# Kernel tuning notes

Measured on AMD Instinct MI355X. Metric: run time of the kernel, lower is better.

The kernel has to match this reference:

```python
import jax, jax.numpy as jnp
import numpy as np

B, S, D, DK = 8, 2048, 768, 214
DROPOUT_P = 0.1


def setup_inputs() -> dict:
    key = jax.random.key(0)
    ks = jax.random.split(key, 11)
    x1 = jax.random.normal(ks[0], (B, S, D), jnp.float32)
    x2 = jax.random.normal(ks[1], (B, S, D), jnp.float32)
    x3 = jax.random.normal(ks[2], (B, S, D), jnp.float32)
    Wq = jax.random.normal(ks[3], (DK, D), jnp.float32) * (1.0 / np.sqrt(D))
    bq = jax.random.normal(ks[4], (DK,), jnp.float32) * 0.01
    Wk = jax.random.normal(ks[5], (DK, D), jnp.float32) * (1.0 / np.sqrt(D))
    bk = jax.random.normal(ks[6], (DK,), jnp.float32) * 0.01
    Wv = jax.random.normal(ks[7], (D, D), jnp.float32) * (1.0 / np.sqrt(D))
    bv = jax.random.normal(ks[8], (D,), jnp.float32) * 0.01
    # full-tensor elementwise divisor: uniform(0,1) + 1, as in the source
    inv_scale = jax.random.uniform(ks[9], (S, S), jnp.float32) + 1.0
    # deterministic inverted-dropout mask, keep prob = 1 - p
    keep = 1.0 - DROPOUT_P
    dropout_mask = (jax.random.uniform(ks[10], (B, S, S)) < keep).astype(jnp.float32) / keep
    return dict(x1=x1, x2=x2, x3=x3, Wq=Wq, bq=bq, Wk=Wk, bk=bk,
                Wv=Wv, bv=bv, inv_scale=inv_scale, dropout_mask=dropout_mask)


def reference(x1, x2, x3, Wq, bq, Wk, bk, Wv, bv, inv_scale, dropout_mask):
    q = jnp.einsum('bsd,kd->bsk', x1, Wq) + bq          # [B,S,DK]
    k = jnp.einsum('bsd,kd->bsk', x2, Wk) + bk          # [B,S,DK]
    v = jnp.einsum('bsd,ed->bse', x3, Wv) + bv          # [B,S,D]
    attn = jnp.einsum('bsk,btk->bst', q, k)             # [B,S,S]
    scaled = attn / inv_scale                           # elementwise full-tensor divisor
    p = jax.nn.softmax(scaled, axis=-1) * dropout_mask  # softmax + inverted dropout
    return jnp.einsum('bst,btd->bsd', p, v)             # [B,S,D]
```

## Files before the change

kernel.cpp:

```cpp
#include <hip/hip_runtime.h>
#include <hip/hip_bf16.h>

typedef unsigned short ushort;
typedef short bf16x8 __attribute__((ext_vector_type(8)));
typedef float f32x4 __attribute__((ext_vector_type(4)));

#define NB 8
#define SS 2048
#define DD 768
#define DKV 214
#define DKP 224
#define WROWS 256
#define MSHIFT 40.0f

__device__ __forceinline__ float bf2f(ushort u) {
  union { unsigned int i; float f; } v; v.i = ((unsigned int)u) << 16; return v.f;
}
__device__ __forceinline__ ushort f2bf(float f) {
  union { float f; unsigned int i; } v; v.f = f;
  unsigned int x = v.i;
  return (ushort)((x + 0x7fffu + ((x >> 16) & 1u)) >> 16);
}
__device__ __forceinline__ void split8v(f32x4 a, f32x4 b, bf16x8& h, bf16x8& l) {
#pragma unroll
  for (int j = 0; j < 4; ++j) {
    ushort h0 = f2bf(a[j]); h[j]     = (short)h0; l[j]     = (short)f2bf(a[j] - bf2f(h0));
    ushort h1 = f2bf(b[j]); h[j + 4] = (short)h1; l[j + 4] = (short)f2bf(b[j] - bf2f(h1));
  }
}
__device__ __forceinline__ bf16x8 cvt8v(f32x4 a, f32x4 b) {
  bf16x8 r;
#pragma unroll
  for (int j = 0; j < 4; ++j) { r[j] = (short)f2bf(a[j]); r[j + 4] = (short)f2bf(b[j]); }
  return r;
}
__device__ __forceinline__ void gload16(const void* g, void* l) {
  __builtin_amdgcn_global_load_lds(
      (const __attribute__((address_space(1))) void*)g,
      (__attribute__((address_space(3))) void*)l, 16, 0, 0);
}

__global__ __launch_bounds__(256)
void prep_w(const float* __restrict__ Wq, const float* __restrict__ Wk,
            const float* __restrict__ Wv,
            ushort* __restrict__ Wqh, ushort* __restrict__ Wql,
            ushort* __restrict__ Wkh, ushort* __restrict__ Wkl,
            ushort* __restrict__ Wvb, float* __restrict__ Z)
{
  const int NW = WROWS * DD;
  const int NV = DD * DD;
  for (int i = blockIdx.x * 256 + threadIdx.x; i < NB * SS; i += gridDim.x * 256)
    Z[i] = 0.f;
  for (int i = blockIdx.x * 256 + threadIdx.x; i < 2 * NW + NV; i += gridDim.x * 256) {
    if (i < NW) {
      int r = i / DD, c = i % DD;
      float v = (r < DKV) ? Wq[i] : 0.f;
      ushort h = f2bf(v);
      int d = (c >> 5) * (WROWS * 32) + r * 32 + (c & 31);
      Wqh[d] = h; Wql[d] = f2bf(v - bf2f(h));
    } else if (i < 2 * NW) {
      int j = i - NW;
      int r = j / DD, c = j % DD;
      float v = (r < DKV) ? Wk[j] : 0.f;
      ushort h = f2bf(v);
      int d = (c >> 5) * (WROWS * 32) + r * 32 + (c & 31);
      Wkh[d] = h; Wkl[d] = f2bf(v - bf2f(h));
    } else {
      int j = i - 2 * NW;
      int r = j / DD, c = j % DD;
      Wvb[(c >> 5) * (DD * 32) + r * 32 + (c & 31)] = f2bf(Wv[j]);
    }
  }
}

__global__ __launch_bounds__(256, 4)
void gemm_qk(const float* __restrict__ x1, const float* __restrict__ x2,
             const ushort* __restrict__ Wqh, const ushort* __restrict__ Wql,
             const ushort* __restrict__ Wkh, const ushort* __restrict__ Wkl,
             const float* __restrict__ bq, const float* __restrict__ bk,
             ushort* __restrict__ Qph, ushort* __restrict__ Qpl,
             ushort* __restrict__ Kph, ushort* __restrict__ Kpl)
{
  const int m0 = blockIdx.x * 64;
  const int which = blockIdx.y >> 1;
  const int n0 = (blockIdx.y & 1) * 128;
  const int tid = threadIdx.x;
  const int w  = tid >> 6;
  const int l  = tid & 63;
  const int lr = l & 15;
  const int lh = l >> 4;

  const float*  A    = which ? x2 : x1;
  const ushort* Bh   = which ? Wkh : Wqh;
  const ushort* Bl   = which ? Wkl : Wql;
  const float*  bias = which ? bk : bq;
  ushort* Ch = which ? Kph : Qph;
  ushort* Cl = which ? Kpl : Qpl;

  __shared__ __align__(16) char lds[2][2][128][64];

  const int srow = (w << 4) + (l >> 2);
  const size_t gc = (size_t)srow * 64 + (size_t)((((l & 3) ^ ((srow >> 1) & 3))) << 4);
  const char* gbh = (const char*)Bh + (size_t)n0 * 64;
  const char* gbl = (const char*)Bl + (size_t)n0 * 64;

  const f32x4 fzero = {0.f, 0.f, 0.f, 0.f};
  f32x4 acc[8];
#pragma unroll
  for (int nt = 0; nt < 8; ++nt) acc[nt] = fzero;

  const float* arow = A + (size_t)(m0 + w * 16 + lr) * DD + lh * 8;

#define QKSTAGE(buf, kk) do {                                             \
    size_t ko = (size_t)(kk) * (WROWS * 64);                              \
    gload16(gbh + ko + gc,        &lds[buf][0][w << 4][0]);               \
    gload16(gbh + ko + gc + 4096, &lds[buf][0][(w << 4) + 64][0]);        \
    gload16(gbl + ko + gc,        &lds[buf][1][w << 4][0]);               \
    gload16(gbl + ko + gc + 4096, &lds[buf][1][(w << 4) + 64][0]);        \
  } while (0)

  QKSTAGE(0, 0);
  f32x4 pa = *(const f32x4*)(arow);
  f32x4 pb = *(const f32x4*)(arow + 4);
  __syncthreads();

  for (int kk = 0; kk < 24; ++kk) {
    const int buf = kk & 1;
    if (kk < 23) QKSTAGE(buf ^ 1, kk + 1);
    f32x4 na = fzero, nb = fzero;
    if (kk < 23) {
      na = *(const f32x4*)(arow + (kk + 1) * 32);
      nb = *(const f32x4*)(arow + (kk + 1) * 32 + 4);
    }
    bf16x8 ah, al; split8v(pa, pb, ah, al);
#pragma unroll
    for (int nt = 0; nt < 8; ++nt) {
      int br = nt * 16 + lr;
      int bo = (lh ^ ((br >> 1) & 3)) << 4;
      bf16x8 wh = *(const bf16x8*)&lds[buf][0][br][bo];
      bf16x8 wl = *(const bf16x8*)&lds[buf][1][br][bo];
      acc[nt] = __builtin_amdgcn_mfma_f32_16x16x32_bf16(ah, wh, acc[nt], 0, 0, 0);
      acc[nt] = __builtin_amdgcn_mfma_f32_16x16x32_bf16(ah, wl, acc[nt], 0, 0, 0);
      acc[nt] = __builtin_amdgcn_mfma_f32_16x16x32_bf16(al, wh, acc[nt], 0, 0, 0);
    }
    __syncthreads();
    pa = na; pb = nb;
  }
#undef QKSTAGE

#pragma unroll
  for (int nt = 0; nt < 8; ++nt) {
    int n = n0 + nt * 16 + lr;
    if (n >= DKP) continue;
    float bv = (n < DKV) ? bias[n] : 0.f;
#pragma unroll
    for (int r = 0; r < 4; ++r) {
      int m = m0 + w * 16 + lh * 4 + r;
      int bb = m >> 11, s = m & 2047;
      float val = (n < DKV) ? (acc[nt][r] + bv) : 0.f;
      ushort h = f2bf(val);
      size_t idx = ((size_t)(bb * 7 + (n >> 5)) * SS + s) * 32 + (n & 31);
      Ch[idx] = h;
      Cl[idx] = f2bf(val - bf2f(h));
    }
  }
}

__global__ __launch_bounds__(256, 3)
void gemm_v(const float* __restrict__ A, const ushort* __restrict__ Bw,
            const float* __restrict__ bias, ushort* __restrict__ Vp)
{
  const int m0 = blockIdx.x * 64;
  const int n0 = blockIdx.y * 256;
  const int tid = threadIdx.x;
  const int w  = tid >> 6;
  const int l  = tid & 63;
  const int lr = l & 15;
  const int lh = l >> 4;

  __shared__ __align__(16) char smem[36864];
  typedef char VBuf[256][64];
  VBuf* stage = (VBuf*)smem;
  ushort (*lt)[72] = (ushort(*)[72])smem;

  const int srow = (w << 4) + (l >> 2);
  const size_t gc = (size_t)srow * 64 + (size_t)((((l & 3) ^ ((srow >> 1) & 3))) << 4);
  const char* gvw = (const char*)Bw + (size_t)n0 * 64;

  const f32x4 fzero = {0.f, 0.f, 0.f, 0.f};
  f32x4 acc[16];
#pragma unroll
  for (int nt = 0; nt < 16; ++nt) acc[nt] = fzero;

  const float* arow = A + (size_t)(m0 + w * 16 + lr) * DD + lh * 8;

#define VSTAGE(buf, kk) do {                                              \
    size_t ko = (size_t)(kk) * (DD * 64);                                 \
    gload16(gvw + ko + gc,         &stage[buf][w << 4][0]);               \
    gload16(gvw + ko + gc + 4096,  &stage[buf][(w << 4) + 64][0]);        \
    gload16(gvw + ko + gc + 8192,  &stage[buf][(w << 4) + 128][0]);       \
    gload16(gvw + ko + gc + 12288, &stage[buf][(w << 4) + 192][0]);       \
  } while (0)

  VSTAGE(0, 0);
  f32x4 pa = *(const f32x4*)(arow);
  f32x4 pb = *(const f32x4*)(arow + 4);
  __syncthreads();

  for (int kk = 0; kk < 24; ++kk) {
    const int buf = kk & 1;
    if (kk < 23) VSTAGE(buf ^ 1, kk + 1);
    f32x4 na = fzero, nb = fzero;
    if (kk < 23) {
      na = *(const f32x4*)(arow + (kk + 1) * 32);
      nb = *(const f32x4*)(arow + (kk + 1) * 32 + 4);
    }
    bf16x8 af = cvt8v(pa, pb);
#pragma unroll
    for (int nt = 0; nt < 16; ++nt) {
      int br = nt * 16 + lr;
      int bo = (lh ^ ((br >> 1) & 3)) << 4;
      bf16x8 bfr = *(const bf16x8*)&stage[buf][br][bo];
      acc[nt] = __builtin_amdgcn_mfma_f32_16x16x32_bf16(af, bfr, acc[nt], 0, 0, 0);
    }
    __syncthreads();
    pa = na; pb = nb;
  }
#undef VSTAGE

#pragma unroll
  for (int nt = 0; nt < 16; ++nt) {
    int nl = nt * 16 + lr;
    float bv = bias[n0 + nl];
#pragma unroll
    for (int r = 0; r < 4; ++r)
      lt[nl][w * 16 + lh * 4 + r] = f2bf(acc[nt][r] + bv);
  }
  __syncthreads();
  const int bb = m0 >> 11;
  const int s0 = m0 & 2047;
  for (int i = tid; i < 256 * 64; i += 256) {
    int nn = i >> 6, mm = i & 63;
    int d = n0 + nn, t = s0 + mm;
    Vp[((size_t)(bb * 64 + (t >> 5)) * DD + d) * 32 + (t & 31)] = lt[nn][mm];
  }
}

__global__ __launch_bounds__(512, 4)
void gemm_s(const ushort* __restrict__ Qph, const ushort* __restrict__ Qpl,
            const ushort* __restrict__ Kph, const ushort* __restrict__ Kpl,
            const float* __restrict__ isc, const float* __restrict__ dmask,
            ushort* __restrict__ Pp, float* __restrict__ Z)
{
  const int bid = blockIdx.x;
  const int bb = bid & 7;
  const int tt = bid >> 3;
  const int m0 = (tt & 15) * 128;
  const int n0 = (tt >> 4) * 256;
  const int tid = threadIdx.x;
  const int w  = tid >> 6;
  const int l  = tid & 63;
  const int lr = l & 15;
  const int lh = l >> 4;
  const int wm = w & 1;
  const int wn = w >> 1;

  __shared__ __align__(16) char Qhb[128][64];
  __shared__ __align__(16) char Qlb[128][64];
  __shared__ __align__(16) char Khb[256][64];
  __shared__ __align__(16) char Klb[256][64];

  const int srow = (w << 4) + (l >> 2);
  const size_t gc = (size_t)srow * 64 + (size_t)((((l & 3) ^ ((srow >> 1) & 3))) << 4);

  const char* gqh = (const char*)Qph + ((size_t)(bb * 7) * SS + m0) * 64;
  const char* gql = (const char*)Qpl + ((size_t)(bb * 7) * SS + m0) * 64;
  const char* gkh = (const char*)Kph + ((size_t)(bb * 7) * SS + n0) * 64;
  const char* gkl = (const char*)Kpl + ((size_t)(bb * 7) * SS + n0) * 64;

  const f32x4 fzero = {0.f, 0.f, 0.f, 0.f};
  f32x4 acc[4][4];
#pragma unroll
  for (int mf = 0; mf < 4; ++mf)
#pragma unroll
    for (int nf = 0; nf < 4; ++nf) acc[mf][nf] = fzero;

#define SSTAGE(kk) do {                                                 \
    size_t ko = (size_t)(kk) * (SS * 64);                               \
    gload16(gqh + ko + gc,        &Qhb[w << 4][0]);                     \
    gload16(gql + ko + gc,        &Qlb[w << 4][0]);                     \
    gload16(gkh + ko + gc,        &Khb[w << 4][0]);                     \
    gload16(gkh + ko + gc + 8192, &Khb[(w << 4) + 128][0]);             \
    gload16(gkl + ko + gc,        &Klb[w << 4][0]);                     \
    gload16(gkl + ko + gc + 8192, &Klb[(w << 4) + 128][0]);             \
  } while (0)

  SSTAGE(0);
  __syncthreads();
#pragma unroll 1
  for (int t = 0; t < 7; ++t) {
    bf16x8 bh[4], bl[4];
#pragma unroll
    for (int nf = 0; nf < 4; ++nf) {
      int br = wn * 64 + nf * 16 + lr;
      int bo = (lh ^ ((br >> 1) & 3)) << 4;
      bh[nf] = *(const bf16x8*)&Khb[br][bo];
      bl[nf] = *(const bf16x8*)&Klb[br][bo];
    }
#pragma unroll
    for (int mf = 0; mf < 4; ++mf) {
      int ar = wm * 64 + mf * 16 + lr;
      int ao = (lh ^ ((ar >> 1) & 3)) << 4;
      bf16x8 ah = *(const bf16x8*)&Qhb[ar][ao];
      bf16x8 al = *(const bf16x8*)&Qlb[ar][ao];
#pragma unroll
      for (int nf = 0; nf < 4; ++nf) {
        acc[mf][nf] = __builtin_amdgcn_mfma_f32_16x16x32_bf16(ah, bh[nf], acc[mf][nf], 0, 0, 0);
        acc[mf][nf] = __builtin_amdgcn_mfma_f32_16x16x32_bf16(ah, bl[nf], acc[mf][nf], 0, 0, 0);
        acc[mf][nf] = __builtin_amdgcn_mfma_f32_16x16x32_bf16(al, bh[nf], acc[mf][nf], 0, 0, 0);
      }
    }
    __syncthreads();
    if (t < 6) {
      SSTAGE(t + 1);
      __syncthreads();
    }
  }
#undef SSTAGE

#pragma unroll
  for (int mf = 0; mf < 4; ++mf) {
#pragma unroll
    for (int r = 0; r < 4; ++r) {
      const int sr = m0 + wm * 64 + mf * 16 + lh * 4 + r;
      float z = 0.f;
#pragma unroll
      for (int nf = 0; nf < 4; ++nf) {
        const int tc = n0 + wn * 64 + nf * 16 + lr;
        float iv = isc[(size_t)sr * SS + tc];
        float sval = acc[mf][nf][r] * __builtin_amdgcn_rcpf(iv);
        float e = __expf(sval - MSHIFT);
        z += e;
        float mk = dmask[(size_t)bb * SS * SS + (size_t)sr * SS + tc];
        Pp[((size_t)(bb * 64 + (tc >> 5)) * SS + sr) * 32 + (tc & 31)] = f2bf(e * mk);
      }
#pragma unroll
      for (int off = 1; off < 16; off <<= 1) z += __shfl_xor(z, off);
      if (lr == 0) atomicAdd(&Z[bb * SS + sr], z);
    }
  }
}

__global__ __launch_bounds__(256, 4)
void gemm_pv(const ushort* __restrict__ Pp, const ushort* __restrict__ Vp,
             const float* __restrict__ Z, float* __restrict__ out)
{
  const int bid = blockIdx.x;
  const int bb = bid & 7;
  const int tt = bid >> 3;
  const int m0 = (tt & 15) * 128;
  const int n0 = (tt >> 4) * 128;
  const int tid = threadIdx.x;
  const int w  = tid >> 6;
  const int l  = tid & 63;
  const int lr = l & 15;
  const int lh = l >> 4;
  const int wm = w & 1;
  const int wn = w >> 1;

  __shared__ __align__(16) char Plb[2][128][64];
  __shared__ __align__(16) char Vlb[2][128][64];

  const int srow = (w << 4) + (l >> 2);
  const size_t gc = (size_t)srow * 64 + (size_t)((((l & 3) ^ ((srow >> 1) & 3))) << 4);

  const char* gpb = (const char*)Pp + ((size_t)(bb * 64) * SS + m0) * 64;
  const char* gvb = (const char*)Vp + ((size_t)(bb * 64) * DD + n0) * 64;

  const f32x4 fzero = {0.f, 0.f, 0.f, 0.f};
  f32x4 acc[4][4];
#pragma unroll
  for (int mf = 0; mf < 4; ++mf)
#pragma unroll
    for (int nf = 0; nf < 4; ++nf) acc[mf][nf] = fzero;

#define PVSTAGE(t) do {                                                   \
    size_t k0 = (size_t)(t) * 2;                                          \
    gload16(gpb + k0 * (SS * 64) + gc,              &Plb[0][w << 4][0]);  \
    gload16(gpb + k0 * (SS * 64) + gc + 4096,       &Plb[0][(w << 4) + 64][0]); \
    gload16(gpb + (k0 + 1) * (SS * 64) + gc,        &Plb[1][w << 4][0]);  \
    gload16(gpb + (k0 + 1) * (SS * 64) + gc + 4096, &Plb[1][(w << 4) + 64][0]); \
    gload16(gvb + k0 * (DD * 64) + gc,              &Vlb[0][w << 4][0]);  \
    gload16(gvb + k0 * (DD * 64) + gc + 4096,       &Vlb[0][(w << 4) + 64][0]); \
    gload16(gvb + (k0 + 1) * (DD * 64) + gc,        &Vlb[1][w << 4][0]);  \
    gload16(gvb + (k0 + 1) * (DD * 64) + gc + 4096, &Vlb[1][(w << 4) + 64][0]); \
  } while (0)

  PVSTAGE(0);
  __syncthreads();
#pragma unroll 1
  for (int t = 0; t < 32; ++t) {
#pragma unroll
    for (int pk = 0; pk < 2; ++pk) {
      bf16x8 bfr[4];
#pragma unroll
      for (int nf = 0; nf < 4; ++nf) {
        int br = wn * 64 + nf * 16 + lr;
        int bo = (lh ^ ((br >> 1) & 3)) << 4;
        bfr[nf] = *(const bf16x8*)&Vlb[pk][br][bo];
      }
#pragma unroll
      for (int mf = 0; mf < 4; ++mf) {
        int ar = wm * 64 + mf * 16 + lr;
        int ao = (lh ^ ((ar >> 1) & 3)) << 4;
        bf16x8 af = *(const bf16x8*)&Plb[pk][ar][ao];
#pragma unroll
        for (int nf = 0; nf < 4; ++nf)
          acc[mf][nf] = __builtin_amdgcn_mfma_f32_16x16x32_bf16(af, bfr[nf], acc[mf][nf], 0, 0, 0);
      }
    }
    __syncthreads();
    if (t < 31) {
      PVSTAGE(t + 1);
      __syncthreads();
    }
  }
#undef PVSTAGE

#pragma unroll
  for (int mf = 0; mf < 4; ++mf) {
#pragma unroll
    for (int r = 0; r < 4; ++r) {
      const int sr = m0 + wm * 64 + mf * 16 + lh * 4 + r;
      float rz = __builtin_amdgcn_rcpf(Z[bb * SS + sr]);
#pragma unroll
      for (int nf = 0; nf < 4; ++nf) {
        const int dc = n0 + wn * 64 + nf * 16 + lr;
        out[((size_t)bb * SS + sr) * DD + dc] = acc[mf][nf][r] * rz;
      }
    }
  }
}

extern "C" void kernel_launch(void* const* d_in, const int* in_sizes, int n_in,
                              void* d_out, int out_size, void* d_ws, size_t ws_size,
                              hipStream_t stream) {
  const float* x1  = (const float*)d_in[0];
  const float* x2  = (const float*)d_in[1];
  const float* x3  = (const float*)d_in[2];
  const float* Wq  = (const float*)d_in[3];
  const float* bq  = (const float*)d_in[4];
  const float* Wk  = (const float*)d_in[5];
  const float* bk  = (const float*)d_in[6];
  const float* Wv  = (const float*)d_in[7];
  const float* bv  = (const float*)d_in[8];
  const float* isc = (const float*)d_in[9];
  const float* dmk = (const float*)d_in[10];
  float* out = (float*)d_out;

  const size_t QKN = (size_t)NB * 7 * SS * 32;
  const size_t VPN = (size_t)NB * 64 * DD * 32;
  const size_t WN  = (size_t)WROWS * DD;
  const size_t NV  = (size_t)DD * DD;
  const size_t PPN = (size_t)NB * 64 * SS * 32;

  ushort* Qph = (ushort*)d_ws;
  ushort* Qpl = Qph + QKN;
  ushort* Kph = Qpl + QKN;
  ushort* Kpl = Kph + QKN;
  ushort* Vp  = Kpl + QKN;
  ushort* Wqh = Vp + VPN;
  ushort* Wql = Wqh + WN;
  ushort* Wkh = Wql + WN;
  ushort* Wkl = Wkh + WN;
  ushort* Wvb = Wkl + WN;
  ushort* Pp  = Wvb + NV;
  float*  Zb  = (float*)(Pp + PPN);

  dim3 blk(256);
  prep_w<<<dim3(512), blk, 0, stream>>>(Wq, Wk, Wv, Wqh, Wql, Wkh, Wkl, Wvb, Zb);
  gemm_qk<<<dim3(256, 4), blk, 0, stream>>>(x1, x2, Wqh, Wql, Wkh, Wkl, bq, bk,
                                            Qph, Qpl, Kph, Kpl);
  gemm_v <<<dim3(256, 3), blk, 0, stream>>>(x3, Wvb, bv, Vp);
  gemm_s <<<dim3(1024), dim3(512), 0, stream>>>(Qph, Qpl, Kph, Kpl, isc, dmk, Pp, Zb);
  gemm_pv<<<dim3(768),  dim3(256), 0, stream>>>(Pp, Vp, Zb, out);
}
```

Measured before the change: 273.6 us.

## Use fp16 single MFMA for QK, bit-pack dropout mask, double-buffer score GEMM

Replaces the split-bf16 three-MFMA emulation for Q/K projection and QK^T with single fp16 MFMAs, halving the Q/K workspace and cutting MFMA count. Adds a pass that packs the dropout mask into bits, which the score kernel reads instead of the float mask; the kernel reconstructs the value as a constant 1/0.9. Double-buffers the score GEMM loads. This risks accuracy loss from fp16, and the bit-packing assumes the mask only holds 0 or 1/keep.

```diff
diff --git a/kernel.cpp b/kernel.cpp
--- a/kernel.cpp
+++ b/kernel.cpp
@@ -2,7 +2,9 @@
 #include <hip/hip_bf16.h>
 
 typedef unsigned short ushort;
+typedef unsigned long long u64;
 typedef short bf16x8 __attribute__((ext_vector_type(8)));
+typedef _Float16 f16x8 __attribute__((ext_vector_type(8)));
 typedef float f32x4 __attribute__((ext_vector_type(4)));
 
 #define NB 8
@@ -21,17 +23,19 @@
   unsigned int x = v.i;
   return (ushort)((x + 0x7fffu + ((x >> 16) & 1u)) >> 16);
 }
-__device__ __forceinline__ void split8v(f32x4 a, f32x4 b, bf16x8& h, bf16x8& l) {
-#pragma unroll
-  for (int j = 0; j < 4; ++j) {
-    ushort h0 = f2bf(a[j]); h[j]     = (short)h0; l[j]     = (short)f2bf(a[j] - bf2f(h0));
-    ushort h1 = f2bf(b[j]); h[j + 4] = (short)h1; l[j + 4] = (short)f2bf(b[j] - bf2f(h1));
-  }
+__device__ __forceinline__ ushort f2h(float f) {
+  union { _Float16 h; ushort u; } cv; cv.h = (_Float16)f; return cv.u;
 }
 __device__ __forceinline__ bf16x8 cvt8v(f32x4 a, f32x4 b) {
   bf16x8 r;
 #pragma unroll
   for (int j = 0; j < 4; ++j) { r[j] = (short)f2bf(a[j]); r[j + 4] = (short)f2bf(b[j]); }
+  return r;
+}
+__device__ __forceinline__ f16x8 cvt8h(f32x4 a, f32x4 b) {
+  f16x8 r;
+#pragma unroll
+  for (int j = 0; j < 4; ++j) { r[j] = (_Float16)a[j]; r[j + 4] = (_Float16)b[j]; }
   return r;
 }
 __device__ __forceinline__ void gload16(const void* g, void* l) {
@@ -41,30 +45,44 @@
 }
 
 __global__ __launch_bounds__(256)
+void prep_sm(const float* __restrict__ dmk, u64* __restrict__ dbits,
+             float* __restrict__ Z)
+{
+  const int tid0 = blockIdx.x * 256 + threadIdx.x;
+  const int stride = gridDim.x * 256;
+  for (int i = tid0; i < NB * SS; i += stride) Z[i] = 0.f;
+  const size_t nwords = (size_t)NB * SS * SS / 64;
+  for (size_t wi = tid0; wi < nwords; wi += stride) {
+    const f32x4* p = (const f32x4*)(dmk + wi * 64);
+    u64 m = 0;
+#pragma unroll
+    for (int j = 0; j < 16; ++j) {
+      f32x4 v = p[j];
+#pragma unroll
+      for (int q = 0; q < 4; ++q) m |= (v[q] > 0.5f) ? (1ull << (j * 4 + q)) : 0ull;
+    }
+    dbits[wi] = m;
+  }
+}
+
+__global__ __launch_bounds__(256)
 void prep_w(const float* __restrict__ Wq, const float* __restrict__ Wk,
             const float* __restrict__ Wv,
-            ushort* __restrict__ Wqh, ushort* __restrict__ Wql,
-            ushort* __restrict__ Wkh, ushort* __restrict__ Wkl,
-            ushort* __restrict__ Wvb, float* __restrict__ Z)
+            ushort* __restrict__ Wqp, ushort* __restrict__ Wkp,
+            ushort* __restrict__ Wvb)
 {
   const int NW = WROWS * DD;
   const int NV = DD * DD;
-  for (int i = blockIdx.x * 256 + threadIdx.x; i < NB * SS; i += gridDim.x * 256)
-    Z[i] = 0.f;
   for (int i = blockIdx.x * 256 + threadIdx.x; i < 2 * NW + NV; i += gridDim.x * 256) {
     if (i < NW) {
       int r = i / DD, c = i % DD;
       float v = (r < DKV) ? Wq[i] : 0.f;
-      ushort h = f2bf(v);
-      int d = (c >> 5) * (WROWS * 32) + r * 32 + (c & 31);
-      Wqh[d] = h; Wql[d] = f2bf(v - bf2f(h));
+      Wqp[(c >> 5) * (WROWS * 32) + r * 32 + (c & 31)] = f2h(v);
     } else if (i < 2 * NW) {
       int j = i - NW;
       int r = j / DD, c = j % DD;
       float v = (r < DKV) ? Wk[j] : 0.f;
-      ushort h = f2bf(v);
-      int d = (c >> 5) * (WROWS * 32) + r * 32 + (c & 31);
-      Wkh[d] = h; Wkl[d] = f2bf(v - bf2f(h));
+      Wkp[(c >> 5) * (WROWS * 32) + r * 32 + (c & 31)] = f2h(v);
     } else {
       int j = i - 2 * NW;
       int r = j / DD, c = j % DD;
@@ -75,11 +93,9 @@
 
 __global__ __launch_bounds__(256, 4)
 void gemm_qk(const float* __restrict__ x1, const float* __restrict__ x2,
-             const ushort* __restrict__ Wqh, const ushort* __restrict__ Wql,
-             const ushort* __restrict__ Wkh, const ushort* __restrict__ Wkl,
+             const ushort* __restrict__ Wqp, const ushort* __restrict__ Wkp,
              const float* __restrict__ bq, const float* __restrict__ bk,
-             ushort* __restrict__ Qph, ushort* __restrict__ Qpl,
-             ushort* __restrict__ Kph, ushort* __restrict__ Kpl)
+             ushort* __restrict__ Qp, ushort* __restrict__ Kp)
 {
   const int m0 = blockIdx.x * 64;
   const int which = blockIdx.y >> 1;
@@ -91,18 +107,15 @@
   const int lh = l >> 4;
 
   const float*  A    = which ? x2 : x1;
-  const ushort* Bh   = which ? Wkh : Wqh;
-  const ushort* Bl   = which ? Wkl : Wql;
+  const ushort* Bw   = which ? Wkp : Wqp;
   const float*  bias = which ? bk : bq;
-  ushort* Ch = which ? Kph : Qph;
-  ushort* Cl = which ? Kpl : Qpl;
-
-  __shared__ __align__(16) char lds[2][2][128][64];
+  ushort* Cp = which ? Kp : Qp;
+
+  __shared__ __align__(16) char lds[2][128][64];
 
   const int srow = (w << 4) + (l >> 2);
   const size_t gc = (size_t)srow * 64 + (size_t)((((l & 3) ^ ((srow >> 1) & 3))) << 4);
-  const char* gbh = (const char*)Bh + (size_t)n0 * 64;
-  const char* gbl = (const char*)Bl + (size_t)n0 * 64;
+  const char* gb = (const char*)Bw + (size_t)n0 * 64;
 
   const f32x4 fzero = {0.f, 0.f, 0.f, 0.f};
   f32x4 acc[8];
@@ -113,10 +126,8 @@
 
 #define QKSTAGE(buf, kk) do {                                             \
     size_t ko = (size_t)(kk) * (WROWS * 64);                              \
-    gload16(gbh + ko + gc,        &lds[buf][0][w << 4][0]);               \
-    gload16(gbh + ko + gc + 4096, &lds[buf][0][(w << 4) + 64][0]);        \
-    gload16(gbl + ko + gc,        &lds[buf][1][w << 4][0]);               \
-    gload16(gbl + ko + gc + 4096, &lds[buf][1][(w << 4) + 64][0]);        \
+    gload16(gb + ko + gc,        &lds[buf][w << 4][0]);                   \
+    gload16(gb + ko + gc + 4096, &lds[buf][(w << 4) + 64][0]);            \
   } while (0)
 
   QKSTAGE(0, 0);
@@ -132,16 +143,13 @@
       na = *(const f32x4*)(arow + (kk + 1) * 32);
       nb = *(const f32x4*)(arow + (kk + 1) * 32 + 4);
     }
-    bf16x8 ah, al; split8v(pa, pb, ah, al);
+    f16x8 af = cvt8h(pa, pb);
 #pragma unroll
     for (int nt = 0; nt < 8; ++nt) {
       int br = nt * 16 + lr;
       int bo = (lh ^ ((br >> 1) & 3)) << 4;
-      bf16x8 wh = *(const bf16x8*)&lds[buf][0][br][bo];
-      bf16x8 wl = *(const bf16x8*)&lds[buf][1][br][bo];
-      acc[nt] = __builtin_amdgcn_mfma_f32_16x16x32_bf16(ah, wh, acc[nt], 0, 0, 0);
-      acc[nt] = __builtin_amdgcn_mfma_f32_16x16x32_bf16(ah, wl, acc[nt], 0, 0, 0);
-      acc[nt] = __builtin_amdgcn_mfma_f32_16x16x32_bf16(al, wh, acc[nt], 0, 0, 0);
+      f16x8 wf = *(const f16x8*)&lds[buf][br][bo];
+      acc[nt] = __builtin_amdgcn_mfma_f32_16x16x32_f16(af, wf, acc[nt], 0, 0, 0);
     }
     __syncthreads();
     pa = na; pb = nb;
@@ -158,10 +166,7 @@
       int m = m0 + w * 16 + lh * 4 + r;
       int bb = m >> 11, s = m & 2047;
       float val = (n < DKV) ? (acc[nt][r] + bv) : 0.f;
-      ushort h = f2bf(val);
-      size_t idx = ((size_t)(bb * 7 + (n >> 5)) * SS + s) * 32 + (n & 31);
-      Ch[idx] = h;
-      Cl[idx] = f2bf(val - bf2f(h));
+      Cp[((size_t)(bb * 7 + (n >> 5)) * SS + s) * 32 + (n & 31)] = f2h(val);
     }
   }
 }
@@ -247,9 +252,8 @@
 }
 
 __global__ __launch_bounds__(512, 4)
-void gemm_s(const ushort* __restrict__ Qph, const ushort* __restrict__ Qpl,
-            const ushort* __restrict__ Kph, const ushort* __restrict__ Kpl,
-            const float* __restrict__ isc, const float* __restrict__ dmask,
+void gemm_s(const ushort* __restrict__ Qp, const ushort* __restrict__ Kp,
+            const float* __restrict__ isc, const u64* __restrict__ dbits,
             ushort* __restrict__ Pp, float* __restrict__ Z)
 {
   const int bid = blockIdx.x;
@@ -265,18 +269,14 @@
   const int wm = w & 1;
   const int wn = w >> 1;
 
-  __shared__ __align__(16) char Qhb[128][64];
-  __shared__ __align__(16) char Qlb[128][64];
-  __shared__ __align__(16) char Khb[256][64];
-  __shared__ __align__(16) char Klb[256][64];
+  __shared__ __align__(16) char Qb[2][128][64];
+  __shared__ __align__(16) char Kb[2][256][64];
 
   const int srow = (w << 4) + (l >> 2);
   const size_t gc = (size_t)srow * 64 + (size_t)((((l & 3) ^ ((srow >> 1) & 3))) << 4);
 
-  const char* gqh = (const char*)Qph + ((size_t)(bb * 7) * SS + m0) * 64;
-  const char* gql = (const char*)Qpl + ((size_t)(bb * 7) * SS + m0) * 64;
-  const char* gkh = (const char*)Kph + ((size_t)(bb * 7) * SS + n0) * 64;
-  const char* gkl = (const char*)Kpl + ((size_t)(bb * 7) * SS + n0) * 64;
+  const char* gq = (const char*)Qp + ((size_t)(bb * 7) * SS + m0) * 64;
+  const char* gk = (const char*)Kp + ((size_t)(bb * 7) * SS + n0) * 64;
 
   const f32x4 fzero = {0.f, 0.f, 0.f, 0.f};
   f32x4 acc[4][4];
@@ -285,54 +285,46 @@
 #pragma unroll
     for (int nf = 0; nf < 4; ++nf) acc[mf][nf] = fzero;
 
-#define SSTAGE(kk) do {                                                 \
+#define SSTAGE(buf, kk) do {                                            \
     size_t ko = (size_t)(kk) * (SS * 64);                               \
-    gload16(gqh + ko + gc,        &Qhb[w << 4][0]);                     \
-    gload16(gql + ko + gc,        &Qlb[w << 4][0]);                     \
-    gload16(gkh + ko + gc,        &Khb[w << 4][0]);                     \
-    gload16(gkh + ko + gc + 8192, &Khb[(w << 4) + 128][0]);             \
-    gload16(gkl + ko + gc,        &Klb[w << 4][0]);                     \
-    gload16(gkl + ko + gc + 8192, &Klb[(w << 4) + 128][0]);             \
+    gload16(gq + ko + gc,        &Qb[buf][w << 4][0]);                  \
+    gload16(gk + ko + gc,        &Kb[buf][w << 4][0]);                  \
+    gload16(gk + ko + gc + 8192, &Kb[buf][(w << 4) + 128][0]);          \
   } while (0)
 
-  SSTAGE(0);
+  SSTAGE(0, 0);
   __syncthreads();
 #pragma unroll 1
   for (int t = 0; t < 7; ++t) {
-    bf16x8 bh[4], bl[4];
+    const int buf = t & 1;
+    if (t < 6) SSTAGE(buf ^ 1, t + 1);
+    f16x8 bfr[4];
 #pragma unroll
     for (int nf = 0; nf < 4; ++nf) {
       int br = wn * 64 + nf * 16 + lr;
       int bo = (lh ^ ((br >> 1) & 3)) << 4;
-      bh[nf] = *(const bf16x8*)&Khb[br][bo];
-      bl[nf] = *(const bf16x8*)&Klb[br][bo];
+      bfr[nf] = *(const f16x8*)&Kb[buf][br][bo];
     }
 #pragma unroll
     for (int mf = 0; mf < 4; ++mf) {
       int ar = wm * 64 + mf * 16 + lr;
       int ao = (lh ^ ((ar >> 1) & 3)) << 4;
-      bf16x8 ah = *(const bf16x8*)&Qhb[ar][ao];
-      bf16x8 al = *(const bf16x8*)&Qlb[ar][ao];
-#pragma unroll
-      for (int nf = 0; nf < 4; ++nf) {
-        acc[mf][nf] = __builtin_amdgcn_mfma_f32_16x16x32_bf16(ah, bh[nf], acc[mf][nf], 0, 0, 0);
-        acc[mf][nf] = __builtin_amdgcn_mfma_f32_16x16x32_bf16(ah, bl[nf], acc[mf][nf], 0, 0, 0);
-        acc[mf][nf] = __builtin_amdgcn_mfma_f32_16x16x32_bf16(al, bh[nf], acc[mf][nf], 0, 0, 0);
-      }
+      f16x8 af = *(const f16x8*)&Qb[buf][ar][ao];
+#pragma unroll
+      for (int nf = 0; nf < 4; ++nf)
+        acc[mf][nf] = __builtin_amdgcn_mfma_f32_16x16x32_f16(af, bfr[nf], acc[mf][nf], 0, 0, 0);
     }
     __syncthreads();
-    if (t < 6) {
-      SSTAGE(t + 1);
-      __syncthreads();
-    }
   }
 #undef SSTAGE
 
+  const float KEEPR = 1.0f / 0.9f;
 #pragma unroll
   for (int mf = 0; mf < 4; ++mf) {
 #pragma unroll
     for (int r = 0; r < 4; ++r) {
       const int sr = m0 + wm * 64 + mf * 16 + lh * 4 + r;
+      const u64 wbits = dbits[((size_t)bb * SS + sr) * (SS / 64) + (n0 >> 6) + wn];
       float z = 0.f;
 #pragma unroll
       for (int nf = 0; nf < 4; ++nf) {
@@ -341,8 +333,8 @@
         float sval = acc[mf][nf][r] * __builtin_amdgcn_rcpf(iv);
         float e = __expf(sval - MSHIFT);
         z += e;
-        float mk = dmask[(size_t)bb * SS * SS + (size_t)sr * SS + tc];
-        Pp[((size_t)(bb * 64 + (tc >> 5)) * SS + sr) * 32 + (tc & 31)] = f2bf(e * mk);
+        float pm = ((wbits >> (nf * 16 + lr)) & 1ull) ? (e * KEEPR) : 0.f;
+        Pp[((size_t)(bb * 64 + (tc >> 5)) * SS + sr) * 32 + (tc & 31)] = f2bf(pm);
       }
 #pragma unroll
       for (int off = 1; off < 16; off <<= 1) z += __shfl_xor(z, off);
@@ -464,24 +456,21 @@
   const size_t NV  = (size_t)DD * DD;
   const size_t PPN = (size_t)NB * 64 * SS * 32;
 
-  ushort* Qph = (ushort*)d_ws;
-  ushort* Qpl = Qph + QKN;
-  ushort* Kph = Qpl + QKN;
-  ushort* Kpl = Kph + QKN;
-  ushort* Vp  = Kpl + QKN;
-  ushort* Wqh = Vp + VPN;
-  ushort* Wql = Wqh + WN;
-  ushort* Wkh = Wql + WN;
-  ushort* Wkl = Wkh + WN;
-  ushort* Wvb = Wkl + WN;
+  ushort* Qp  = (ushort*)d_ws;
+  ushort* Kp  = Qp + QKN;
+  ushort* Vp  = Kp + QKN;
+  ushort* Wqp = Vp + VPN;
+  ushort* Wkp = Wqp + WN;
+  ushort* Wvb = Wkp + WN;
   ushort* Pp  = Wvb + NV;
   float*  Zb  = (float*)(Pp + PPN);
+  u64*    dbits = (u64*)(Zb + NB * SS);
 
   dim3 blk(256);
-  prep_w<<<dim3(512), blk, 0, stream>>>(Wq, Wk, Wv, Wqh, Wql, Wkh, Wkl, Wvb, Zb);
-  gemm_qk<<<dim3(256, 4), blk, 0, stream>>>(x1, x2, Wqh, Wql, Wkh, Wkl, bq, bk,
-                                            Qph, Qpl, Kph, Kpl);
+  prep_w<<<dim3(512),  blk, 0, stream>>>(Wq, Wk, Wv, Wqp, Wkp, Wvb);
+  prep_sm<<<dim3(2048), blk, 0, stream>>>(dmk, dbits, Zb);
+  gemm_qk<<<dim3(256, 4), blk, 0, stream>>>(x1, x2, Wqp, Wkp, bq, bk, Qp, Kp);
   gemm_v <<<dim3(256, 3), blk, 0, stream>>>(x3, Wvb, bv, Vp);
-  gemm_s <<<dim3(1024), dim3(512), 0, stream>>>(Qph, Qpl, Kph, Kpl, isc, dmk, Pp, Zb);
+  gemm_s <<<dim3(1024), dim3(512), 0, stream>>>(Qp, Kp, isc, dbits, Pp, Zb);
   gemm_pv<<<dim3(768),  dim3(256), 0, stream>>>(Pp, Vp, Zb, out);
 }
```

New measurement: 263.1 us. -3.8%, faster.
